# Kernel tuning notes

Hardware: AMD Instinct MI355X
Metric: run time of the kernel (lower is better)

## Reference

```python
import jax, jax.numpy as jnp
import numpy as np
from jax import lax

ALPHA = 0.85
C1 = 0.01 ** 2
C2 = 0.03 ** 2


def _avg_pool3(x):
    # F.avg_pool2d(x, 3, 1, 1) with count_include_pad=True: zero-pad, divide by 9.
    s = lax.reduce_window(x, jnp.array(0.0, x.dtype), lax.add,
                          (1, 1, 3, 3), (1, 1, 1, 1),
                          [(0, 0), (0, 0), (1, 1), (1, 1)])
    return s / jnp.array(9.0, x.dtype)


def _ssim(x, y):
    mu_x = _avg_pool3(x)
    mu_y = _avg_pool3(y)
    sigma_x = jnp.clip(_avg_pool3(x * x) - mu_x * mu_x, 0.0, None)
    sigma_y = jnp.clip(_avg_pool3(y * y) - mu_y * mu_y, 0.0, None)
    sigma_xy = _avg_pool3(x * y) - mu_x * mu_y
    ssim_n = (2.0 * mu_x * mu_y + C1) * (2.0 * sigma_xy + C2)
    ssim_d = (mu_x * mu_x + mu_y * mu_y + C1) * (sigma_x + sigma_y + C2)
    return jnp.clip((1.0 - ssim_n / ssim_d) / 2.0, 0.0, 1.0)


def _warp_right(right_img, disp):
    # grid_sample(bilinear, border, align_corners=True) where y maps identically
    # to its own row -> a 1D horizontal bilinear gather at x_sample = x - disp.
    B, C, H, W = right_img.shape
    x_base = jnp.arange(W, dtype=disp.dtype).reshape(1, 1, 1, W)
    x_sample = x_base - disp                      # [B,1,H,W]
    xs = jnp.clip(x_sample, 0.0, W - 1.0)         # border padding
    x0 = jnp.floor(xs)
    w = xs - x0                                   # frac weight
    i0 = x0.astype(jnp.int32)
    i1 = jnp.minimum(i0 + 1, W - 1)
    i0b = jnp.broadcast_to(i0, (B, C, H, W))
    i1b = jnp.broadcast_to(i1, (B, C, H, W))
    g0 = jnp.take_along_axis(right_img, i0b, axis=3)
    g1 = jnp.take_along_axis(right_img, i1b, axis=3)
    warped = (1.0 - w) * g0 + w * g1              # w broadcasts over C
    valid = ((x_sample > 0) & (x_sample < W - 1)).astype(disp.dtype)
    return warped, valid


def setup_inputs() -> dict:
    key = jax.random.key(0)
    k1, k2, k3 = jax.random.split(key, 3)
    B, H, W = 8, 720, 1280
    disp = jax.random.normal(k1, (B, 1, H, W), dtype=jnp.float32)
    left_img = jax.random.uniform(k2, (B, 3, H, W), dtype=jnp.float32)
    right_img = jax.random.uniform(k3, (B, 3, H, W), dtype=jnp.float32)
    return {"disp": disp, "left_img": left_img, "right_img": right_img}


def reference(disp, left_img, right_img):
    right_warped, valid = _warp_right(right_img, disp)
    l1_err = jnp.mean(jnp.abs(left_img - right_warped), axis=1, keepdims=True)
    ssim_err = jnp.mean(_ssim(left_img, right_warped), axis=1, keepdims=True)
    photo_err = ALPHA * ssim_err + (1.0 - ALPHA) * l1_err
    n_valid = jnp.maximum(jnp.sum(valid), 1.0)
    return jnp.sum(photo_err * valid) / n_valid
```

## Files before the change

### kernel.cpp

```cpp
#include <hip/hip_runtime.h>


#define P_ALPHA 0.85f
#define P_C1 1e-4f
#define P_C2 9e-4f

constexpr int COLS  = 62;
constexpr int RPW   = 12;
constexpr int WAVES = 4;

__global__ __launch_bounds__(256)
void photo_loss_kernel(const float* __restrict__ disp,
                       const float* __restrict__ left,
                       const float* __restrict__ right,
                       float* __restrict__ acc,
                       int H, int W)
{
    __shared__ float redpv[WAVES];
    __shared__ float redv[WAVES];

    const int tid  = threadIdx.x;
    const int lane = tid & 63;
    const int w    = tid >> 6;
    const int b    = blockIdx.z;
    const int col  = blockIdx.x * COLS + lane - 1;
    const int rowStart = (blockIdx.y * WAVES + w) * RPW;

    const int planeHW = H * W;
    const float* __restrict__ dispb = disp  + b * planeHW;
    const float* __restrict__ L0 = left  + (b * 3 + 0) * planeHW;
    const float* __restrict__ L1 = left  + (b * 3 + 1) * planeHW;
    const float* __restrict__ L2 = left  + (b * 3 + 2) * planeHW;
    const float* __restrict__ R0 = right + (b * 3 + 0) * planeHW;
    const float* __restrict__ R1 = right + (b * 3 + 1) * planeHW;
    const float* __restrict__ R2 = right + (b * 3 + 2) * planeHW;

    const float wm1f = (float)(W - 1);
    const int   colC = min(max(col, 0), W - 1);
    const float colv = (col >= 0 && col < W) ? 1.f : 0.f;
    const float ocm  = (lane >= 1 && lane <= COLS && col < W) ? 1.f : 0.f;

    float rsx[3][3], rsy[3][3], rsxx[3][3], rsyy[3][3], rsxy[3][3];
    float l1r[3], vr[3];

    float sum_pv = 0.f, sum_v = 0.f;

    auto emit = [&](int cs) {
        const float inv9 = 1.f / 9.f;
        float ssim_sum = 0.f;
        #pragma unroll
        for (int c = 0; c < 3; ++c) {
            float mu_x = (rsx[c][0]  + rsx[c][1]  + rsx[c][2])  * inv9;
            float mu_y = (rsy[c][0]  + rsy[c][1]  + rsy[c][2])  * inv9;
            float exx  = (rsxx[c][0] + rsxx[c][1] + rsxx[c][2]) * inv9;
            float eyy  = (rsyy[c][0] + rsyy[c][1] + rsyy[c][2]) * inv9;
            float exy  = (rsxy[c][0] + rsxy[c][1] + rsxy[c][2]) * inv9;
            float sig_x  = fmaxf(exx - mu_x * mu_x, 0.f);
            float sig_y  = fmaxf(eyy - mu_y * mu_y, 0.f);
            float sig_xy = exy - mu_x * mu_y;
            float n  = (2.f * mu_x * mu_y + P_C1) * (2.f * sig_xy + P_C2);
            float dd = (mu_x * mu_x + mu_y * mu_y + P_C1) * (sig_x + sig_y + P_C2);
            float s  = (1.f - n * __builtin_amdgcn_rcpf(dd)) * 0.5f;
            s = fminf(fmaxf(s, 0.f), 1.f);
            ssim_sum += s;
        }
        float photo = P_ALPHA * (ssim_sum * (1.f / 3.f))
                    + (1.f - P_ALPHA) * (l1r[cs] * (1.f / 3.f));
        sum_pv += photo * vr[cs] * ocm;
        sum_v  += vr[cs] * ocm;
    };

    float dC, xC0, xC1, xC2;
    {
        const int r  = rowStart - 1;
        const int rc = min(max(r, 0), H - 1);
        const int off = rc * W + colC;
        dC = dispb[off]; xC0 = L0[off]; xC1 = L1[off]; xC2 = L2[off];
    }

    #pragma unroll
    for (int j = 0; j <= RPW + 2; ++j) {
        const int s = j % 3;
        const int r = rowStart - 1 + j;
        if (j <= RPW + 1) {
            const int   rc = min(max(r, 0), H - 1);
            const float rv = (r >= 0 && r < H) ? 1.f : 0.f;
            const float m  = rv * colv;

            const float xs  = (float)col - dC;
            const float xcl = fminf(fmaxf(xs, 0.f), wm1f);
            const float xf  = floorf(xcl);
            const float fr  = xcl - xf;
            const int   i0  = (int)xf;
            const int   i1  = min(i0 + 1, W - 1);
            const int   ro  = rc * W;
            const float g00 = R0[ro + i0], g01 = R0[ro + i1];
            const float g10 = R1[ro + i0], g11 = R1[ro + i1];
            const float g20 = R2[ro + i0], g21 = R2[ro + i1];

            float dN = 0.f, xN0 = 0.f, xN1 = 0.f, xN2 = 0.f;
            if (j <= RPW) {
                const int rn   = min(max(r + 1, 0), H - 1);
                const int offn = rn * W + colC;
                dN = dispb[offn]; xN0 = L0[offn]; xN1 = L1[offn]; xN2 = L2[offn];
            }

            if (j >= 3) emit((s + 1) % 3);

            const float omf = 1.f - fr;
            const float y0 = (omf * g00 + fr * g01) * m;
            const float y1 = (omf * g10 + fr * g11) * m;
            const float y2 = (omf * g20 + fr * g21) * m;
            const float x0 = xC0 * m;
            const float x1 = xC1 * m;
            const float x2 = xC2 * m;

            float xl, xr, yl, yr;
            xl = __shfl_up(x0, 1, 64); xr = __shfl_down(x0, 1, 64);
            yl = __shfl_up(y0, 1, 64); yr = __shfl_down(y0, 1, 64);
            rsx[0][s]  = xl + x0 + xr;
            rsy[0][s]  = yl + y0 + yr;
            rsxx[0][s] = xl * xl + x0 * x0 + xr * xr;
            rsyy[0][s] = yl * yl + y0 * y0 + yr * yr;
            rsxy[0][s] = xl * yl + x0 * y0 + xr * yr;

            xl = __shfl_up(x1, 1, 64); xr = __shfl_down(x1, 1, 64);
            yl = __shfl_up(y1, 1, 64); yr = __shfl_down(y1, 1, 64);
            rsx[1][s]  = xl + x1 + xr;
            rsy[1][s]  = yl + y1 + yr;
            rsxx[1][s] = xl * xl + x1 * x1 + xr * xr;
            rsyy[1][s] = yl * yl + y1 * y1 + yr * yr;
            rsxy[1][s] = xl * yl + x1 * y1 + xr * yr;

            xl = __shfl_up(x2, 1, 64); xr = __shfl_down(x2, 1, 64);
            yl = __shfl_up(y2, 1, 64); yr = __shfl_down(y2, 1, 64);
            rsx[2][s]  = xl + x2 + xr;
            rsy[2][s]  = yl + y2 + yr;
            rsxx[2][s] = xl * xl + x2 * x2 + xr * xr;
            rsyy[2][s] = yl * yl + y2 * y2 + yr * yr;
            rsxy[2][s] = xl * yl + x2 * y2 + xr * yr;

            l1r[s] = fabsf(x0 - y0) + fabsf(x1 - y1) + fabsf(x2 - y2);
            vr[s]  = (xs > 0.f && xs < wm1f) ? 1.f : 0.f;

            dC = dN; xC0 = xN0; xC1 = xN1; xC2 = xN2;
        } else {
            emit((s + 1) % 3);
        }
    }

    #pragma unroll
    for (int off = 32; off > 0; off >>= 1) {
        sum_pv += __shfl_down(sum_pv, off, 64);
        sum_v  += __shfl_down(sum_v,  off, 64);
    }
    if (lane == 0) { redpv[w] = sum_pv; redv[w] = sum_v; }
    __syncthreads();
    if (tid == 0) {
        atomicAdd(&acc[0], redpv[0] + redpv[1] + redpv[2] + redpv[3]);
        atomicAdd(&acc[1], redv[0]  + redv[1]  + redv[2]  + redv[3]);
    }
}

__global__ void photo_loss_finalize(const float* __restrict__ acc,
                                    float* __restrict__ out)
{
    out[0] = acc[0] / fmaxf(acc[1], 1.f);
}

extern "C" void kernel_launch(void* const* d_in, const int* in_sizes, int n_in,
                              void* d_out, int out_size, void* d_ws, size_t ws_size,
                              hipStream_t stream)
{
    const float* disp  = (const float*)d_in[0];
    const float* left  = (const float*)d_in[1];
    const float* right = (const float*)d_in[2];
    float* out = (float*)d_out;
    float* acc = (float*)d_ws;

    const int B = 8, H = 720, W = 1280;

    hipMemsetAsync(acc, 0, 2 * sizeof(float), stream);

    dim3 grid((W + COLS - 1) / COLS, H / (WAVES * RPW), B);
    dim3 block(256);
    photo_loss_kernel<<<grid, block, 0, stream>>>(disp, left, right, acc, H, W);
    photo_loss_finalize<<<1, 1, 0, stream>>>(acc, out);
}
```

Baseline: 244.0 us.

## Software-pipeline disparity and gather loads two rows ahead

Restructures the row loop so the disparity for row r+2 is loaded early, letting the dependent right-image gathers for row r+1 issue one iteration ahead instead of waiting on a disparity load in the same iteration. RPW grows from 12 to 15, so each wave covers more rows and the halo overhead per output row shrinks. The launch bound now requests 4 blocks per CU. The intent is to hide the latency of the dependent gather chain, at the cost of more live registers.

Measured after the change: 239.7 us. No clear change (-1.8%).

```diff
diff --git a/kernel.cpp b/kernel.cpp
--- a/kernel.cpp
+++ b/kernel.cpp
@@ -6,10 +6,10 @@
 #define P_C2 9e-4f
 
 constexpr int COLS  = 62;
-constexpr int RPW   = 12;
+constexpr int RPW   = 15;
 constexpr int WAVES = 4;
 
-__global__ __launch_bounds__(256)
+__global__ __launch_bounds__(256, 4)
 void photo_loss_kernel(const float* __restrict__ disp,
                        const float* __restrict__ left,
                        const float* __restrict__ right,
@@ -70,12 +70,30 @@
         sum_v  += vr[cs] * ocm;
     };
 
-    float dC, xC0, xC1, xC2;
+    float gC0,gC1,gC2,gC3,gC4,gC5, frC, vmC;
+    float xC0,xC1,xC2;
+    float dN;
+    int   offN;
+
     {
-        const int r  = rowStart - 1;
-        const int rc = min(max(r, 0), H - 1);
-        const int off = rc * W + colC;
-        dC = dispb[off]; xC0 = L0[off]; xC1 = L1[off]; xC2 = L2[off];
+        const int r0   = rowStart - 1;
+        const int rc0  = max(r0, 0);
+        const int off0 = rc0 * W + colC;
+        const float d0 = dispb[off0];
+        xC0 = L0[off0]; xC1 = L1[off0]; xC2 = L2[off0];
+        offN = rowStart * W + colC;
+        dN = dispb[offN];
+        const float xs  = (float)col - d0;
+        const float xcl = fminf(fmaxf(xs, 0.f), wm1f);
+        const float xf  = floorf(xcl);
+        frC = xcl - xf;
+        const int i0 = (int)xf;
+        const int i1 = min(i0 + 1, W - 1);
+        const int ro = rc0 * W;
+        gC0 = R0[ro + i0]; gC1 = R0[ro + i1];
+        gC2 = R1[ro + i0]; gC3 = R1[ro + i1];
+        gC4 = R2[ro + i0]; gC5 = R2[ro + i1];
+        vmC = (xs > 0.f && xs < wm1f) ? 1.f : 0.f;
     }
 
     #pragma unroll
@@ -83,34 +101,36 @@
         const int s = j % 3;
         const int r = rowStart - 1 + j;
         if (j <= RPW + 1) {
-            const int   rc = min(max(r, 0), H - 1);
+            float gN0=0.f,gN1=0.f,gN2=0.f,gN3=0.f,gN4=0.f,gN5=0.f, frN=0.f, vmN=0.f;
+            float xN0=0.f,xN1=0.f,xN2=0.f, dF=0.f;
+            int   offF = 0;
+            if (j <= RPW) {
+                const float xs  = (float)col - dN;
+                const float xcl = fminf(fmaxf(xs, 0.f), wm1f);
+                const float xf  = floorf(xcl);
+                frN = xcl - xf;
+                const int i0 = (int)xf;
+                const int i1 = min(i0 + 1, W - 1);
+                const int ro = offN - colC;
+                gN0 = R0[ro + i0]; gN1 = R0[ro + i1];
+                gN2 = R1[ro + i0]; gN3 = R1[ro + i1];
+                gN4 = R2[ro + i0]; gN5 = R2[ro + i1];
+                vmN = (xs > 0.f && xs < wm1f) ? 1.f : 0.f;
+
+                xN0 = L0[offN]; xN1 = L1[offN]; xN2 = L2[offN];
+                const int rc2 = min(r + 2, H - 1);
+                offF = rc2 * W + colC;
+                dF = dispb[offF];
+            }
+
+            if (j >= 3) emit((s + 1) % 3);
+
             const float rv = (r >= 0 && r < H) ? 1.f : 0.f;
             const float m  = rv * colv;
-
-            const float xs  = (float)col - dC;
-            const float xcl = fminf(fmaxf(xs, 0.f), wm1f);
-            const float xf  = floorf(xcl);
-            const float fr  = xcl - xf;
-            const int   i0  = (int)xf;
-            const int   i1  = min(i0 + 1, W - 1);
-            const int   ro  = rc * W;
-            const float g00 = R0[ro + i0], g01 = R0[ro + i1];
-            const float g10 = R1[ro + i0], g11 = R1[ro + i1];
-            const float g20 = R2[ro + i0], g21 = R2[ro + i1];
-
-            float dN = 0.f, xN0 = 0.f, xN1 = 0.f, xN2 = 0.f;
-            if (j <= RPW) {
-                const int rn   = min(max(r + 1, 0), H - 1);
-                const int offn = rn * W + colC;
-                dN = dispb[offn]; xN0 = L0[offn]; xN1 = L1[offn]; xN2 = L2[offn];
-            }
-
-            if (j >= 3) emit((s + 1) % 3);
-
-            const float omf = 1.f - fr;
-            const float y0 = (omf * g00 + fr * g01) * m;
-            const float y1 = (omf * g10 + fr * g11) * m;
-            const float y2 = (omf * g20 + fr * g21) * m;
+            const float omf = 1.f - frC;
+            const float y0 = (omf * gC0 + frC * gC1) * m;
+            const float y1 = (omf * gC2 + frC * gC3) * m;
+            const float y2 = (omf * gC4 + frC * gC5) * m;
             const float x0 = xC0 * m;
             const float x1 = xC1 * m;
             const float x2 = xC2 * m;
@@ -141,9 +161,14 @@
             rsxy[2][s] = xl * yl + x2 * y2 + xr * yr;
 
             l1r[s] = fabsf(x0 - y0) + fabsf(x1 - y1) + fabsf(x2 - y2);
-            vr[s]  = (xs > 0.f && xs < wm1f) ? 1.f : 0.f;
-
-            dC = dN; xC0 = xN0; xC1 = xN1; xC2 = xN2;
+            vr[s]  = vmC;
+
+            if (j <= RPW) {
+                gC0 = gN0; gC1 = gN1; gC2 = gN2; gC3 = gN3; gC4 = gN4; gC5 = gN5;
+                frC = frN; vmC = vmN;
+                xC0 = xN0; xC1 = xN1; xC2 = xN2;
+                dN = dF; offN = offF;
+            }
         } else {
             emit((s + 1) % 3);
         }
```

## Stage right-image row window in registers and gather via wave shuffles

Applied to the files above, without the earlier changes.

Instead of doing scattered global gathers of the right image for the bilinear warp, each lane loads two coalesced 64-wide row windows (offset -8 and +56) per channel, and the warp samples are fetched with ds_bpermute shuffles. If any lane's sample falls outside the 128-column window, that wave falls back to the original global loads. Rows per wave also rise from 12 to 15, which lowers halo overhead but shrinks the grid and raises register pressure. The change also removes row clamps it treats as redundant.

Measured after the change: 284.0 us. +16.4%, slower.

```diff
diff --git a/kernel.cpp b/kernel.cpp
--- a/kernel.cpp
+++ b/kernel.cpp
@@ -6,7 +6,7 @@
 #define P_C2 9e-4f
 
 constexpr int COLS  = 62;
-constexpr int RPW   = 12;
+constexpr int RPW   = 15;
 constexpr int WAVES = 4;
 
 __global__ __launch_bounds__(256)
@@ -23,7 +23,8 @@
     const int lane = tid & 63;
     const int w    = tid >> 6;
     const int b    = blockIdx.z;
-    const int col  = blockIdx.x * COLS + lane - 1;
+    const int s0   = blockIdx.x * COLS;
+    const int col  = s0 + lane - 1;
     const int rowStart = (blockIdx.y * WAVES + w) * RPW;
 
     const int planeHW = H * W;
@@ -36,9 +37,13 @@
     const float* __restrict__ R2 = right + (b * 3 + 2) * planeHW;
 
     const float wm1f = (float)(W - 1);
+    const float colf = (float)col;
     const int   colC = min(max(col, 0), W - 1);
     const float colv = (col >= 0 && col < W) ? 1.f : 0.f;
     const float ocm  = (lane >= 1 && lane <= COLS && col < W) ? 1.f : 0.f;
+
+    const int colA = min(max(s0 - 8  + lane, 0), W - 1);
+    const int colB = min(max(s0 + 56 + lane, 0), W - 1);
 
     float rsx[3][3], rsy[3][3], rsxx[3][3], rsyy[3][3], rsxy[3][3];
     float l1r[3], vr[3];
@@ -71,11 +76,15 @@
     };
 
     float dC, xC0, xC1, xC2;
+    float hA0, hA1, hA2, hB0, hB1, hB2;
     {
-        const int r  = rowStart - 1;
-        const int rc = min(max(r, 0), H - 1);
+        const int rc  = max(rowStart - 1, 0);
         const int off = rc * W + colC;
         dC = dispb[off]; xC0 = L0[off]; xC1 = L1[off]; xC2 = L2[off];
+        const int ro = rc * W;
+        hA0 = R0[ro + colA]; hB0 = R0[ro + colB];
+        hA1 = R1[ro + colA]; hB1 = R1[ro + colB];
+        hA2 = R2[ro + colA]; hB2 = R2[ro + colB];
     }
 
     #pragma unroll
@@ -83,30 +92,62 @@
         const int s = j % 3;
         const int r = rowStart - 1 + j;
         if (j <= RPW + 1) {
-            const int   rc = min(max(r, 0), H - 1);
-            const float rv = (r >= 0 && r < H) ? 1.f : 0.f;
-            const float m  = rv * colv;
-
-            const float xs  = (float)col - dC;
+            float dN = 0.f, xN0 = 0.f, xN1 = 0.f, xN2 = 0.f;
+            float nA0 = 0.f, nA1 = 0.f, nA2 = 0.f, nB0 = 0.f, nB1 = 0.f, nB2 = 0.f;
+            if (j <= RPW) {
+                const int rn   = min(r + 1, H - 1);
+                const int offn = rn * W + colC;
+                dN = dispb[offn]; xN0 = L0[offn]; xN1 = L1[offn]; xN2 = L2[offn];
+                const int ron = rn * W;
+                nA0 = R0[ron + colA]; nB0 = R0[ron + colB];
+                nA1 = R1[ron + colA]; nB1 = R1[ron + colB];
+                nA2 = R2[ron + colA]; nB2 = R2[ron + colB];
+            }
+
+            const float xs  = colf - dC;
             const float xcl = fminf(fmaxf(xs, 0.f), wm1f);
             const float xf  = floorf(xcl);
             const float fr  = xcl - xf;
             const int   i0  = (int)xf;
-            const int   i1  = min(i0 + 1, W - 1);
-            const int   ro  = rc * W;
-            const float g00 = R0[ro + i0], g01 = R0[ro + i1];
-            const float g10 = R1[ro + i0], g11 = R1[ro + i1];
-            const float g20 = R2[ro + i0], g21 = R2[ro + i1];
-
-            float dN = 0.f, xN0 = 0.f, xN1 = 0.f, xN2 = 0.f;
-            if (j <= RPW) {
-                const int rn   = min(max(r + 1, 0), H - 1);
-                const int offn = rn * W + colC;
-                dN = dispb[offn]; xN0 = L0[offn]; xN1 = L1[offn]; xN2 = L2[offn];
+            const int   k   = i0 - s0 + 8;
+            const int   k1  = k + 1;
+            const int   ks  = k & 63;
+            const int   k1s = k1 & 63;
+            float g00, g01, g10, g11, g20, g21;
+            {
+                const float a  = __shfl(hA0, ks, 64),  bb = __shfl(hB0, ks, 64);
+                const float a1 = __shfl(hA0, k1s, 64), b1 = __shfl(hB0, k1s, 64);
+                g00 = (k  < 64) ? a  : bb;
+                g01 = (k1 < 64) ? a1 : b1;
+            }
+            {
+                const float a  = __shfl(hA1, ks, 64),  bb = __shfl(hB1, ks, 64);
+                const float a1 = __shfl(hA1, k1s, 64), b1 = __shfl(hB1, k1s, 64);
+                g10 = (k  < 64) ? a  : bb;
+                g11 = (k1 < 64) ? a1 : b1;
+            }
+            {
+                const float a  = __shfl(hA2, ks, 64),  bb = __shfl(hB2, ks, 64);
+                const float a1 = __shfl(hA2, k1s, 64), b1 = __shfl(hB2, k1s, 64);
+                g20 = (k  < 64) ? a  : bb;
+                g21 = (k1 < 64) ? a1 : b1;
+            }
+            const bool bad = (k < 0) || (k1 > 127);
+            if (__builtin_expect(__any(bad), 0)) {
+                if (bad) {
+                    const int rc = min(max(r, 0), H - 1);
+                    const int ro = rc * W;
+                    const int i1 = min(i0 + 1, W - 1);
+                    g00 = R0[ro + i0]; g01 = R0[ro + i1];
+                    g10 = R1[ro + i0]; g11 = R1[ro + i1];
+                    g20 = R2[ro + i0]; g21 = R2[ro + i1];
+                }
             }
 
             if (j >= 3) emit((s + 1) % 3);
 
+            const float rv  = (r >= 0 && r < H) ? 1.f : 0.f;
+            const float m   = rv * colv;
             const float omf = 1.f - fr;
             const float y0 = (omf * g00 + fr * g01) * m;
             const float y1 = (omf * g10 + fr * g11) * m;
@@ -144,6 +185,8 @@
             vr[s]  = (xs > 0.f && xs < wm1f) ? 1.f : 0.f;
 
             dC = dN; xC0 = xN0; xC1 = xN1; xC2 = xN2;
+            hA0 = nA0; hA1 = nA1; hA2 = nA2;
+            hB0 = nB0; hB1 = nB1; hB2 = nB2;
         } else {
             emit((s + 1) % 3);
         }
```

## Split channels across waves and replace gathered right-image loads with wave shuffles

Applied to the files above, without the earlier changes.

Each of three waves now handles one color channel over a block of rows, instead of each wave processing all three channels for its own rows. The per-pixel bilinear gathers from the right image become two coalesced loads per row (a window from s0-8 to s0+119), and the needed values are fetched with cross-lane shuffles. Any lane whose sample falls outside that window takes a slow path that loads directly from global memory. The aim is to cut uncoalesced gather traffic and register pressure, at the cost of loading disparity redundantly in every wave and doing more shuffles and selects.

New measurement: 381.6 us. 1.56x slower.

```diff
diff --git a/kernel.cpp b/kernel.cpp
--- a/kernel.cpp
+++ b/kernel.cpp
@@ -5,160 +5,130 @@
 #define P_C1 1e-4f
 #define P_C2 9e-4f
 
-constexpr int COLS  = 62;
-constexpr int RPW   = 12;
-constexpr int WAVES = 4;
+constexpr int COLS = 62;
+constexpr int RPW  = 15;
 
-__global__ __launch_bounds__(256)
+__global__ __launch_bounds__(192)
 void photo_loss_kernel(const float* __restrict__ disp,
                        const float* __restrict__ left,
                        const float* __restrict__ right,
                        float* __restrict__ acc,
                        int H, int W)
 {
-    __shared__ float redpv[WAVES];
-    __shared__ float redv[WAVES];
+    __shared__ float redpv[3];
+    __shared__ float redv;
 
     const int tid  = threadIdx.x;
     const int lane = tid & 63;
-    const int w    = tid >> 6;
+    const int c    = tid >> 6;
     const int b    = blockIdx.z;
-    const int col  = blockIdx.x * COLS + lane - 1;
-    const int rowStart = (blockIdx.y * WAVES + w) * RPW;
+    const int s0   = blockIdx.x * COLS;
+    const int col  = s0 + lane - 1;
+    const int rowStart = blockIdx.y * RPW;
 
     const int planeHW = H * W;
     const float* __restrict__ dispb = disp  + b * planeHW;
-    const float* __restrict__ L0 = left  + (b * 3 + 0) * planeHW;
-    const float* __restrict__ L1 = left  + (b * 3 + 1) * planeHW;
-    const float* __restrict__ L2 = left  + (b * 3 + 2) * planeHW;
-    const float* __restrict__ R0 = right + (b * 3 + 0) * planeHW;
-    const float* __restrict__ R1 = right + (b * 3 + 1) * planeHW;
-    const float* __restrict__ R2 = right + (b * 3 + 2) * planeHW;
+    const float* __restrict__ X = left  + (b * 3 + c) * planeHW;
+    const float* __restrict__ R = right + (b * 3 + c) * planeHW;
 
     const float wm1f = (float)(W - 1);
+    const float colf = (float)col;
     const int   colC = min(max(col, 0), W - 1);
     const float colv = (col >= 0 && col < W) ? 1.f : 0.f;
     const float ocm  = (lane >= 1 && lane <= COLS && col < W) ? 1.f : 0.f;
 
-    float rsx[3][3], rsy[3][3], rsxx[3][3], rsyy[3][3], rsxy[3][3];
-    float l1r[3], vr[3];
+    const int colA = min(max(s0 - 8  + lane, 0), W - 1);
+    const int colB = min(max(s0 + 56 + lane, 0), W - 1);
+
+    float Ax=0.f, Ay=0.f, Axx=0.f, Ayy=0.f, Axy=0.f;
+    float Bx=0.f, By=0.f, Bxx=0.f, Byy=0.f, Bxy=0.f;
+    float l1B=0.f, vB=0.f;
 
     float sum_pv = 0.f, sum_v = 0.f;
 
-    auto emit = [&](int cs) {
-        const float inv9 = 1.f / 9.f;
-        float ssim_sum = 0.f;
-        #pragma unroll
-        for (int c = 0; c < 3; ++c) {
-            float mu_x = (rsx[c][0]  + rsx[c][1]  + rsx[c][2])  * inv9;
-            float mu_y = (rsy[c][0]  + rsy[c][1]  + rsy[c][2])  * inv9;
-            float exx  = (rsxx[c][0] + rsxx[c][1] + rsxx[c][2]) * inv9;
-            float eyy  = (rsyy[c][0] + rsyy[c][1] + rsyy[c][2]) * inv9;
-            float exy  = (rsxy[c][0] + rsxy[c][1] + rsxy[c][2]) * inv9;
-            float sig_x  = fmaxf(exx - mu_x * mu_x, 0.f);
-            float sig_y  = fmaxf(eyy - mu_y * mu_y, 0.f);
-            float sig_xy = exy - mu_x * mu_y;
-            float n  = (2.f * mu_x * mu_y + P_C1) * (2.f * sig_xy + P_C2);
-            float dd = (mu_x * mu_x + mu_y * mu_y + P_C1) * (sig_x + sig_y + P_C2);
-            float s  = (1.f - n * __builtin_amdgcn_rcpf(dd)) * 0.5f;
+    #pragma unroll 2
+    for (int j = 0; j < RPW + 2; ++j) {
+        const int r  = rowStart - 1 + j;
+        const int rc = min(max(r, 0), H - 1);
+        const float rv = (r >= 0 && r < H) ? 1.f : 0.f;
+
+        const int   off = rc * W + colC;
+        const float d   = dispb[off];
+        const float xc  = X[off];
+        const int   ro  = rc * W;
+        const float hA  = R[ro + colA];
+        const float hB  = R[ro + colB];
+
+        const float xs  = colf - d;
+        const float xcl = fminf(fmaxf(xs, 0.f), wm1f);
+        const float xf  = floorf(xcl);
+        const float fr  = xcl - xf;
+        const int   i0  = (int)xf;
+        const int   k   = i0 - s0 + 8;
+        const int   k1  = k + 1;
+        float g0, g1;
+        {
+            const float a  = __shfl(hA, k  & 63, 64), bb = __shfl(hB, k  & 63, 64);
+            const float a1 = __shfl(hA, k1 & 63, 64), b1 = __shfl(hB, k1 & 63, 64);
+            g0 = (k  < 64) ? a  : bb;
+            g1 = (k1 < 64) ? a1 : b1;
+        }
+        const bool bad = (k < 0) || (k1 > 127);
+        if (__builtin_expect(__any(bad), 0)) {
+            if (bad) {
+                const int i1 = min(i0 + 1, W - 1);
+                g0 = R[ro + i0]; g1 = R[ro + i1];
+            }
+        }
+
+        const float m  = rv * colv;
+        const float y  = ((1.f - fr) * g0 + fr * g1) * m;
+        const float x  = xc * m;
+        const float xl = __shfl_up(x, 1, 64), xr = __shfl_down(x, 1, 64);
+        const float yl = __shfl_up(y, 1, 64), yr = __shfl_down(y, 1, 64);
+        const float Cx  = xl + x + xr;
+        const float Cy  = yl + y + yr;
+        const float Cxx = xl*xl + x*x + xr*xr;
+        const float Cyy = yl*yl + y*y + yr*yr;
+        const float Cxy = xl*yl + x*y + xr*yr;
+        const float l1C = fabsf(x - y);
+        const float vC  = (xs > 0.f && xs < wm1f) ? 1.f : 0.f;
+
+        if (j >= 2) {
+            const float inv9 = 1.f / 9.f;
+            const float mu_x = (Ax  + Bx  + Cx)  * inv9;
+            const float mu_y = (Ay  + By  + Cy)  * inv9;
+            const float exx  = (Axx + Bxx + Cxx) * inv9;
+            const float eyy  = (Ayy + Byy + Cyy) * inv9;
+            const float exy  = (Axy + Bxy + Cxy) * inv9;
+            const float sig_x  = fmaxf(exx - mu_x * mu_x, 0.f);
+            const float sig_y  = fmaxf(eyy - mu_y * mu_y, 0.f);
+            const float sig_xy = exy - mu_x * mu_y;
+            const float n  = (2.f * mu_x * mu_y + P_C1) * (2.f * sig_xy + P_C2);
+            const float dd = (mu_x * mu_x + mu_y * mu_y + P_C1) * (sig_x + sig_y + P_C2);
+            float s = (1.f - n * __builtin_amdgcn_rcpf(dd)) * 0.5f;
             s = fminf(fmaxf(s, 0.f), 1.f);
-            ssim_sum += s;
+            const float photo_c = (P_ALPHA * (1.f / 3.f)) * s
+                                + ((1.f - P_ALPHA) * (1.f / 3.f)) * l1B;
+            sum_pv += photo_c * vB * ocm;
+            sum_v  += vB * ocm;
         }
-        float photo = P_ALPHA * (ssim_sum * (1.f / 3.f))
-                    + (1.f - P_ALPHA) * (l1r[cs] * (1.f / 3.f));
-        sum_pv += photo * vr[cs] * ocm;
-        sum_v  += vr[cs] * ocm;
-    };
 
-    float dC, xC0, xC1, xC2;
-    {
-        const int r  = rowStart - 1;
-        const int rc = min(max(r, 0), H - 1);
-        const int off = rc * W + colC;
-        dC = dispb[off]; xC0 = L0[off]; xC1 = L1[off]; xC2 = L2[off];
+        Ax = Bx; Ay = By; Axx = Bxx; Ayy = Byy; Axy = Bxy;
+        Bx = Cx; By = Cy; Bxx = Cxx; Byy = Cyy; Bxy = Cxy;
+        l1B = l1C; vB = vC;
     }
 
     #pragma unroll
-    for (int j = 0; j <= RPW + 2; ++j) {
-        const int s = j % 3;
-        const int r = rowStart - 1 + j;
-        if (j <= RPW + 1) {
-            const int   rc = min(max(r, 0), H - 1);
-            const float rv = (r >= 0 && r < H) ? 1.f : 0.f;
-            const float m  = rv * colv;
-
-            const float xs  = (float)col - dC;
-            const float xcl = fminf(fmaxf(xs, 0.f), wm1f);
-            const float xf  = floorf(xcl);
-            const float fr  = xcl - xf;
-            const int   i0  = (int)xf;
-            const int   i1  = min(i0 + 1, W - 1);
-            const int   ro  = rc * W;
-            const float g00 = R0[ro + i0], g01 = R0[ro + i1];
-            const float g10 = R1[ro + i0], g11 = R1[ro + i1];
-            const float g20 = R2[ro + i0], g21 = R2[ro + i1];
-
-            float dN = 0.f, xN0 = 0.f, xN1 = 0.f, xN2 = 0.f;
-            if (j <= RPW) {
-                const int rn   = min(max(r + 1, 0), H - 1);
-                const int offn = rn * W + colC;
-                dN = dispb[offn]; xN0 = L0[offn]; xN1 = L1[offn]; xN2 = L2[offn];
-            }
-
-            if (j >= 3) emit((s + 1) % 3);
-
-            const float omf = 1.f - fr;
-            const float y0 = (omf * g00 + fr * g01) * m;
-            const float y1 = (omf * g10 + fr * g11) * m;
-            const float y2 = (omf * g20 + fr * g21) * m;
-            const float x0 = xC0 * m;
-            const float x1 = xC1 * m;
-            const float x2 = xC2 * m;
-
-            float xl, xr, yl, yr;
-            xl = __shfl_up(x0, 1, 64); xr = __shfl_down(x0, 1, 64);
-            yl = __shfl_up(y0, 1, 64); yr = __shfl_down(y0, 1, 64);
-            rsx[0][s]  = xl + x0 + xr;
-            rsy[0][s]  = yl + y0 + yr;
-            rsxx[0][s] = xl * xl + x0 * x0 + xr * xr;
-            rsyy[0][s] = yl * yl + y0 * y0 + yr * yr;
-            rsxy[0][s] = xl * yl + x0 * y0 + xr * yr;
-
-            xl = __shfl_up(x1, 1, 64); xr = __shfl_down(x1, 1, 64);
-            yl = __shfl_up(y1, 1, 64); yr = __shfl_down(y1, 1, 64);
-            rsx[1][s]  = xl + x1 + xr;
-            rsy[1][s]  = yl + y1 + yr;
-            rsxx[1][s] = xl * xl + x1 * x1 + xr * xr;
-            rsyy[1][s] = yl * yl + y1 * y1 + yr * yr;
-            rsxy[1][s] = xl * yl + x1 * y1 + xr * yr;
-
-            xl = __shfl_up(x2, 1, 64); xr = __shfl_down(x2, 1, 64);
-            yl = __shfl_up(y2, 1, 64); yr = __shfl_down(y2, 1, 64);
-            rsx[2][s]  = xl + x2 + xr;
-            rsy[2][s]  = yl + y2 + yr;
-            rsxx[2][s] = xl * xl + x2 * x2 + xr * xr;
-            rsyy[2][s] = yl * yl + y2 * y2 + yr * yr;
-            rsxy[2][s] = xl * yl + x2 * y2 + xr * yr;
-
-            l1r[s] = fabsf(x0 - y0) + fabsf(x1 - y1) + fabsf(x2 - y2);
-            vr[s]  = (xs > 0.f && xs < wm1f) ? 1.f : 0.f;
-
-            dC = dN; xC0 = xN0; xC1 = xN1; xC2 = xN2;
-        } else {
-            emit((s + 1) % 3);
-        }
+    for (int o = 32; o > 0; o >>= 1) {
+        sum_pv += __shfl_down(sum_pv, o, 64);
+        sum_v  += __shfl_down(sum_v,  o, 64);
     }
-
-    #pragma unroll
-    for (int off = 32; off > 0; off >>= 1) {
-        sum_pv += __shfl_down(sum_pv, off, 64);
-        sum_v  += __shfl_down(sum_v,  off, 64);
-    }
-    if (lane == 0) { redpv[w] = sum_pv; redv[w] = sum_v; }
+    if (lane == 0) { redpv[c] = sum_pv; if (c == 0) redv = sum_v; }
     __syncthreads();
     if (tid == 0) {
-        atomicAdd(&acc[0], redpv[0] + redpv[1] + redpv[2] + redpv[3]);
-        atomicAdd(&acc[1], redv[0]  + redv[1]  + redv[2]  + redv[3]);
+        atomicAdd(&acc[0], redpv[0] + redpv[1] + redpv[2]);
+        atomicAdd(&acc[1], redv);
     }
 }
 
@@ -182,8 +152,8 @@
 
     hipMemsetAsync(acc, 0, 2 * sizeof(float), stream);
 
-    dim3 grid((W + COLS - 1) / COLS, H / (WAVES * RPW), B);
-    dim3 block(256);
+    dim3 grid((W + COLS - 1) / COLS, H / RPW, B);
+    dim3 block(192);
     photo_loss_kernel<<<grid, block, 0, stream>>>(disp, left, right, acc, H, W);
     photo_loss_finalize<<<1, 1, 0, stream>>>(acc, out);
 }
```
